# Performance work log

Hardware: AMD Instinct MI355X
Metric: run time of the kernel (lower is better)

## Reference

```python
import jax, jax.numpy as jnp
import numpy as np

D_IN = 1024
D_ATT = 1024
D_OUT = 1024
N, S = 8, 4096


def setup_inputs() -> dict:
    key = jax.random.key(0)
    ks = jax.random.split(key, 5)
    sc_in = 1.0 / np.sqrt(D_IN)
    sc_att = 1.0 / np.sqrt(D_ATT)
    return {
        "x": jax.random.normal(ks[0], (N, S, D_IN), dtype=jnp.float32),
        "Wq": jax.random.normal(ks[1], (D_IN, D_ATT), dtype=jnp.float32) * sc_in,
        "bq": jnp.zeros((D_ATT,), dtype=jnp.float32),
        "Wk": jax.random.normal(ks[2], (D_IN, D_ATT), dtype=jnp.float32) * sc_in,
        "bk": jnp.zeros((D_ATT,), dtype=jnp.float32),
        "Wv": jax.random.normal(ks[3], (D_IN, D_ATT), dtype=jnp.float32) * sc_in,
        "bv": jnp.zeros((D_ATT,), dtype=jnp.float32),
        "Wo": jax.random.normal(ks[4], (D_ATT, D_OUT), dtype=jnp.float32) * sc_att,
        "bo": jnp.zeros((D_OUT,), dtype=jnp.float32),
    }


def reference(x, Wq, bq, Wk, bk, Wv, bv, Wo, bo):
    # projections: [n, s, h]
    query = jnp.einsum('nsd,dh->nsh', x, Wq) + bq
    keyp = jnp.einsum('nsd,dh->nsh', x, Wk) + bk
    value = jnp.einsum('nsd,dh->nsh', x, Wv) + bv
    fmap = lambda t: jax.nn.elu(t) + 1.0
    Q = fmap(query)
    K = fmap(keyp)
    # per-channel reductions over sequence: [n, h]
    KV = jnp.sum(K * value, axis=1)
    Ksum = jnp.sum(K, axis=1)
    Z = 1.0 / (Q * Ksum[:, None, :] + 1e-6)  # [n, s, h]
    V = Q * KV[:, None, :] * Z  # [n, s, h]
    out = jnp.einsum('nsh,ho->nso', V, Wo) + bo
    return jax.nn.gelu(out)  # flax nn.gelu default approximate=True
```

## Files before the change

kernel.cpp:

```cpp
#include <hip/hip_runtime.h>
#include <hip/hip_bf16.h>

typedef __attribute__((ext_vector_type(8))) short bf16x8;
typedef __attribute__((ext_vector_type(4))) float f32x4;

#define GLOBAL_AS __attribute__((address_space(1)))
#define LDS_AS __attribute__((address_space(3)))

#define DCH 1024
#define SEQ 4096
#define NBATCH 8

static __device__ __forceinline__ unsigned int f2bf(float f) {
    unsigned int u = __float_as_uint(f);
    return (u + 0x7fffu + ((u >> 16) & 1u)) >> 16;
}

static __device__ __forceinline__ void async_copy16(const void* g, void* l) {
    __builtin_amdgcn_global_load_lds((const GLOBAL_AS void*)g, (LDS_AS void*)l, 16, 0, 0);
}

static __device__ __forceinline__ float gelu_tanh(float u) {
    float inner = 0.7978845608028654f * (u + 0.044715f * u * u * u);
    return 0.5f * u * (1.f + tanhf(inner));
}

__global__ __launch_bounds__(256) void prep_kernel(
    const float4* __restrict__ x, uint4* __restrict__ xb,
    const float* __restrict__ Wk, const float* __restrict__ Wv,
    unsigned short* __restrict__ WkT, unsigned short* __restrict__ WvT)
{
    __shared__ float tile[32][33];
    int tid = threadIdx.x;
    if (blockIdx.x < 16384) {
        size_t t = (size_t)blockIdx.x * 256 + tid;
        float4 f0 = x[t * 2], f1 = x[t * 2 + 1];
        uint4 a;
        a.x = f2bf(f0.x) | (f2bf(f0.y) << 16);
        a.y = f2bf(f0.z) | (f2bf(f0.w) << 16);
        a.z = f2bf(f1.x) | (f2bf(f1.y) << 16);
        a.w = f2bf(f1.z) | (f2bf(f1.w) << 16);
        xb[t] = a;
    } else {
        int b2 = blockIdx.x - 16384;
        const float* src = (b2 >> 10) ? Wv : Wk;
        unsigned short* dst = (b2 >> 10) ? WvT : WkT;
        int h0 = (b2 & 31) * 32, k0 = ((b2 >> 5) & 31) * 32;
        int tx = tid & 31, ty = tid >> 5;
#pragma unroll
        for (int i = 0; i < 4; i++)
            tile[ty + i * 8][tx] = src[(size_t)(k0 + ty + i * 8) * DCH + h0 + tx];
        __syncthreads();
#pragma unroll
        for (int i = 0; i < 4; i++)
            dst[(size_t)(h0 + ty + i * 8) * DCH + k0 + tx] =
                (unsigned short)f2bf(tile[tx][ty + i * 8]);
    }
}

__global__ __launch_bounds__(256) void wt_kernel(
    const float* __restrict__ Wk, const float* __restrict__ Wv,
    unsigned short* __restrict__ WkT, unsigned short* __restrict__ WvT)
{
    __shared__ float tile[32][33];
    const float* src = blockIdx.z ? Wv : Wk;
    unsigned short* dst = blockIdx.z ? WvT : WkT;
    int h0 = blockIdx.x * 32, k0 = blockIdx.y * 32;
    int tx = threadIdx.x, ty = threadIdx.y;
#pragma unroll
    for (int i = 0; i < 4; i++)
        tile[ty + i * 8][tx] = src[(size_t)(k0 + ty + i * 8) * DCH + h0 + tx];
    __syncthreads();
#pragma unroll
    for (int i = 0; i < 4; i++)
        dst[(size_t)(h0 + ty + i * 8) * DCH + k0 + tx] =
            (unsigned short)f2bf(tile[tx][ty + i * 8]);
}

__global__ __launch_bounds__(256) void kv_gemm_fast(
    const unsigned short* __restrict__ xb,
    const unsigned short* __restrict__ WkT,
    const unsigned short* __restrict__ WvT,
    const float* __restrict__ bk,
    const float* __restrict__ bv,
    float* __restrict__ part)
{
    __shared__ __align__(16) unsigned short sA[2][128 * 64];
    __shared__ __align__(16) unsigned short sK[2][64 * 64];
    __shared__ __align__(16) unsigned short sV[2][64 * 64];

    int b = blockIdx.x;
    int r = b & 7, j = b >> 3;
    int h_tile = j & 15;
    int ns = r * 32 + (j >> 4);
    int n = ns >> 5, s_tile = ns & 31;
    int s0 = s_tile * 128, h0 = h_tile * 64;

    int tid = threadIdx.x;
    int lane = tid & 63, wid = tid >> 6;
    int wsg = wid >> 1, wh = wid & 1;
    int col = lane & 15, lhi = lane >> 4;

    const unsigned short* gA[4];
    int aoff[4];
#pragma unroll
    for (int i = 0; i < 4; i++) {
        int c = (wid * 4 + i) * 64 + lane;
        int row = c >> 3, c8 = (c & 7) ^ (row & 7);
        gA[i] = xb + (size_t)(n * SEQ + s0 + row) * DCH + c8 * 8;
        aoff[i] = (wid * 4 + i) * 512;
    }
    const unsigned short* gK[2];
    const unsigned short* gV[2];
    int koff[2];
#pragma unroll
    for (int i = 0; i < 2; i++) {
        int c = (wid * 2 + i) * 64 + lane;
        int row = c >> 3, c8 = (c & 7) ^ (row & 7);
        gK[i] = WkT + (size_t)(h0 + row) * DCH + c8 * 8;
        gV[i] = WvT + (size_t)(h0 + row) * DCH + c8 * 8;
        koff[i] = (wid * 2 + i) * 512;
    }

    f32x4 acck[4][2], accv[4][2];
#pragma unroll
    for (int mt = 0; mt < 4; mt++)
#pragma unroll
        for (int nt = 0; nt < 2; nt++) {
            acck[mt][nt] = (f32x4){0.f, 0.f, 0.f, 0.f};
            accv[mt][nt] = (f32x4){0.f, 0.f, 0.f, 0.f};
        }

#pragma unroll
    for (int i = 0; i < 4; i++) async_copy16(gA[i], &sA[0][aoff[i]]);
#pragma unroll
    for (int i = 0; i < 2; i++) async_copy16(gK[i], &sK[0][koff[i]]);
#pragma unroll
    for (int i = 0; i < 2; i++) async_copy16(gV[i], &sV[0][koff[i]]);
    __syncthreads();

    int cur = 0;
    for (int kk = 0; kk < 16; kk++) {
        if (kk < 15) {
            int k0 = (kk + 1) * 64;
#pragma unroll
            for (int i = 0; i < 4; i++) async_copy16(gA[i] + k0, &sA[cur ^ 1][aoff[i]]);
#pragma unroll
            for (int i = 0; i < 2; i++) async_copy16(gK[i] + k0, &sK[cur ^ 1][koff[i]]);
#pragma unroll
            for (int i = 0; i < 2; i++) async_copy16(gV[i] + k0, &sV[cur ^ 1][koff[i]]);
        }
#pragma unroll
        for (int ks = 0; ks < 2; ks++) {
            bf16x8 af[4], bkf[2], bvf[2];
            int gg = ks * 4 + lhi;
#pragma unroll
            for (int mt = 0; mt < 4; mt++) {
                int rowa = wsg * 64 + mt * 16 + col;
                af[mt] = *((const bf16x8*)&sA[cur][rowa * 64 + ((gg ^ (rowa & 7)) * 8)]);
            }
#pragma unroll
            for (int nt = 0; nt < 2; nt++) {
                int rowb = wh * 32 + nt * 16 + col;
                int o = rowb * 64 + ((gg ^ (rowb & 7)) * 8);
                bkf[nt] = *((const bf16x8*)&sK[cur][o]);
                bvf[nt] = *((const bf16x8*)&sV[cur][o]);
            }
            __builtin_amdgcn_s_setprio(1);
#pragma unroll
            for (int mt = 0; mt < 4; mt++)
#pragma unroll
                for (int nt = 0; nt < 2; nt++) {
                    acck[mt][nt] = __builtin_amdgcn_mfma_f32_16x16x32_bf16(
                        af[mt], bkf[nt], acck[mt][nt], 0, 0, 0);
                    accv[mt][nt] = __builtin_amdgcn_mfma_f32_16x16x32_bf16(
                        af[mt], bvf[nt], accv[mt][nt], 0, 0, 0);
                }
            __builtin_amdgcn_s_setprio(0);
        }
        __syncthreads();
        cur ^= 1;
    }

    float* redf = (float*)&sA[0][0];

#pragma unroll
    for (int nt = 0; nt < 2; nt++) {
        int h_local = wh * 32 + nt * 16 + col;
        float bkv = bk[h0 + h_local];
        float bvv = bv[h0 + h_local];
        float pkv = 0.f, pks = 0.f;
#pragma unroll
        for (int mt = 0; mt < 4; mt++)
#pragma unroll
            for (int rr = 0; rr < 4; rr++) {
                float ck = acck[mt][nt][rr] + bkv;
                float cv = accv[mt][nt][rr] + bvv;
                float kq = ck > 0.f ? ck + 1.f : __expf(ck);
                pkv += kq * cv;
                pks += kq;
            }
        pkv += __shfl_xor(pkv, 16);
        pkv += __shfl_xor(pkv, 32);
        pks += __shfl_xor(pks, 16);
        pks += __shfl_xor(pks, 32);
        if (lhi == 0) {
            redf[(wsg * 64 + h_local) * 2 + 0] = pkv;
            redf[(wsg * 64 + h_local) * 2 + 1] = pks;
        }
    }
    __syncthreads();
    if (tid < 128) {
        int h = tid & 63, t = tid >> 6;
        float v = redf[(h) * 2 + t] + redf[(64 + h) * 2 + t];
        part[(((size_t)(n * 16 + h_tile) * 2 + t) * 32 + s_tile) * 64 + h] = v;
    }
}

__global__ __launch_bounds__(512) void kv_gemm_slow(
    const float* __restrict__ x,
    const unsigned short* __restrict__ WkT,
    const unsigned short* __restrict__ WvT,
    const float* __restrict__ bk,
    const float* __restrict__ bv,
    float* __restrict__ part)
{
    __shared__ unsigned short sA[128 * 64];
    __shared__ unsigned short sK[128 * 64];
    __shared__ unsigned short sV[128 * 64];
    __shared__ float red[2][128][2];

    int b = blockIdx.x;
    int r = b & 7, j = b >> 3;
    int ns = r * 32 + (j >> 3);
    int h_tile = j & 7;
    int n = ns >> 5, s_tile = ns & 31;
    int s0 = s_tile * 128, h0 = h_tile * 128;

    const float* xA = x + ((size_t)(n * SEQ + s0)) * DCH;

    int tid = threadIdx.x;
    int lane = tid & 63, wid = tid >> 6;
    int wsg = wid >> 2, wh = wid & 3;
    int col = lane & 15, lhi = lane >> 4;

    f32x4 acck[4][2], accv[4][2];
#pragma unroll
    for (int mt = 0; mt < 4; mt++)
#pragma unroll
        for (int nt = 0; nt < 2; nt++) {
            acck[mt][nt] = (f32x4){0.f, 0.f, 0.f, 0.f};
            accv[mt][nt] = (f32x4){0.f, 0.f, 0.f, 0.f};
        }

    for (int kk = 0; kk < 16; kk++) {
        int k0 = kk * 64;
#pragma unroll
        for (int i = 0; i < 2; i++) {
            int c = tid + i * 512;
            int row = c >> 3, c8 = c & 7;
            const float4* p = (const float4*)(xA + (size_t)row * DCH + k0 + c8 * 8);
            float4 f0 = p[0], f1 = p[1];
            unsigned int p0 = f2bf(f0.x) | (f2bf(f0.y) << 16);
            unsigned int p1 = f2bf(f0.z) | (f2bf(f0.w) << 16);
            unsigned int p2 = f2bf(f1.x) | (f2bf(f1.y) << 16);
            unsigned int p3 = f2bf(f1.z) | (f2bf(f1.w) << 16);
            uint4 pk = {p0, p1, p2, p3};
            int g = c8 ^ (row & 7);
            *((uint4*)&sA[row * 64 + g * 8]) = pk;
        }
#pragma unroll
        for (int i = 0; i < 2; i++) {
            int c = tid + i * 512;
            int row = c >> 3, c8 = c & 7;
            int g = c8 ^ (row & 7);
            *((uint4*)&sK[row * 64 + g * 8]) =
                *((const uint4*)(WkT + (size_t)(h0 + row) * DCH + k0 + c8 * 8));
            *((uint4*)&sV[row * 64 + g * 8]) =
                *((const uint4*)(WvT + (size_t)(h0 + row) * DCH + k0 + c8 * 8));
        }
        __syncthreads();
#pragma unroll
        for (int ks = 0; ks < 2; ks++) {
            bf16x8 af[4], bkf[2], bvf[2];
            int gg = ks * 4 + lhi;
#pragma unroll
            for (int mt = 0; mt < 4; mt++) {
                int rowa = wsg * 64 + mt * 16 + col;
                af[mt] = *((const bf16x8*)&sA[rowa * 64 + ((gg ^ (rowa & 7)) * 8)]);
            }
#pragma unroll
            for (int nt = 0; nt < 2; nt++) {
                int rowb = wh * 32 + nt * 16 + col;
                int o = rowb * 64 + ((gg ^ (rowb & 7)) * 8);
                bkf[nt] = *((const bf16x8*)&sK[o]);
                bvf[nt] = *((const bf16x8*)&sV[o]);
            }
#pragma unroll
            for (int mt = 0; mt < 4; mt++)
#pragma unroll
                for (int nt = 0; nt < 2; nt++) {
                    acck[mt][nt] = __builtin_amdgcn_mfma_f32_16x16x32_bf16(
                        af[mt], bkf[nt], acck[mt][nt], 0, 0, 0);
                    accv[mt][nt] = __builtin_amdgcn_mfma_f32_16x16x32_bf16(
                        af[mt], bvf[nt], accv[mt][nt], 0, 0, 0);
                }
        }
        __syncthreads();
    }

#pragma unroll
    for (int nt = 0; nt < 2; nt++) {
        int h_local = wh * 32 + nt * 16 + col;
        float bkv = bk[h0 + h_local];
        float bvv = bv[h0 + h_local];
        float pkv = 0.f, pks = 0.f;
#pragma unroll
        for (int mt = 0; mt < 4; mt++)
#pragma unroll
            for (int rr = 0; rr < 4; rr++) {
                float ck = acck[mt][nt][rr] + bkv;
                float cv = accv[mt][nt][rr] + bvv;
                float kq = ck > 0.f ? ck + 1.f : __expf(ck);
                pkv += kq * cv;
                pks += kq;
            }
        pkv += __shfl_xor(pkv, 16);
        pkv += __shfl_xor(pkv, 32);
        pks += __shfl_xor(pks, 16);
        pks += __shfl_xor(pks, 32);
        if (lhi == 0) {
            red[wsg][h_local][0] = pkv;
            red[wsg][h_local][1] = pks;
        }
    }
    __syncthreads();
    if (tid < 256) {
        int h = tid & 127, t = tid >> 7;
        float v = red[0][h][t] + red[1][h][t];
        int ht = h_tile * 2 + (h >> 6);
        part[(((size_t)(n * 16 + ht) * 2 + t) * 32 + s_tile) * 64 + (h & 63)] = v;
    }
}

__global__ __launch_bounds__(256) void out_part_kernel(
    const float* __restrict__ part, const float* __restrict__ Wo,
    float* __restrict__ part2)
{
    __shared__ float skv[128], sks[128], vs[128];
    int n = blockIdx.x, kc = blockIdx.y, ob = blockIdx.z;
    int tid = threadIdx.x;
    {
        int h = tid & 127, t = tid >> 7;
        int ht = kc * 2 + (h >> 6);
        const float* base = part + (((size_t)(n * 16 + ht) * 2 + t) * 32) * 64;
        float s = 0.f;
#pragma unroll 4
        for (int st = 0; st < 32; st++) s += base[st * 64 + (h & 63)];
        if (t == 0) skv[h] = s; else sks[h] = s;
    }
    __syncthreads();
    if (tid < 128) vs[tid] = skv[tid] / sks[tid];
    __syncthreads();
    int o = ob * 256 + tid;
    float acc = 0.f;
#pragma unroll 8
    for (int k = 0; k < 128; k++)
        acc += vs[k] * Wo[(size_t)(kc * 128 + k) * DCH + o];
    part2[(size_t)(n * 8 + kc) * DCH + o] = acc;
}

__global__ __launch_bounds__(256) void bcast_kernel(
    const float4* __restrict__ part2, const float4* __restrict__ bo,
    float4* __restrict__ out)
{
    int n = blockIdx.x >> 7;
    int sc = blockIdx.x & 127;
    int tid = threadIdx.x;
    float4 a = bo[tid];
#pragma unroll
    for (int kc = 0; kc < 8; kc++) {
        float4 p = part2[(size_t)(n * 8 + kc) * 256 + tid];
        a.x += p.x; a.y += p.y; a.z += p.z; a.w += p.w;
    }
    float4 v;
    v.x = gelu_tanh(a.x);
    v.y = gelu_tanh(a.y);
    v.z = gelu_tanh(a.z);
    v.w = gelu_tanh(a.w);
    size_t base = ((size_t)(n * SEQ) + (size_t)sc * 32) * 256 + tid;
#pragma unroll 4
    for (int s = 0; s < 32; s++)
        out[base + (size_t)s * 256] = v;
}

extern "C" void kernel_launch(void* const* d_in, const int* in_sizes, int n_in,
                              void* d_out, int out_size, void* d_ws, size_t ws_size,
                              hipStream_t stream) {
    const float* x  = (const float*)d_in[0];
    const float* Wk = (const float*)d_in[3];
    const float* bk = (const float*)d_in[4];
    const float* Wv = (const float*)d_in[5];
    const float* bv = (const float*)d_in[6];
    const float* Wo = (const float*)d_in[7];
    const float* bo = (const float*)d_in[8];

    const size_t XB_BYTES = (size_t)NBATCH * SEQ * DCH * 2;
    const size_t TAIL = (4u << 20) + (8u << 20) + (1u << 19);
    bool fast = ws_size >= XB_BYTES + TAIL;

    char* ws = (char*)d_ws;
    unsigned short* xb = (unsigned short*)ws;
    char* base = fast ? ws + XB_BYTES : ws;
    unsigned short* WkT = (unsigned short*)base;
    unsigned short* WvT = WkT + 1024 * 1024;
    float* part  = (float*)(base + 4 * 1024 * 1024);
    float* part2 = part + (size_t)8 * 16 * 2 * 32 * 64;

    if (fast) {
        prep_kernel<<<18432, 256, 0, stream>>>((const float4*)x, (uint4*)xb,
                                               Wk, Wv, WkT, WvT);
        kv_gemm_fast<<<4096, 256, 0, stream>>>(xb, WkT, WvT, bk, bv, part);
    } else {
        wt_kernel<<<dim3(32, 32, 2), dim3(32, 8), 0, stream>>>(Wk, Wv, WkT, WvT);
        kv_gemm_slow<<<2048, 512, 0, stream>>>(x, WkT, WvT, bk, bv, part);
    }
    out_part_kernel<<<dim3(8, 8, 4), 256, 0, stream>>>(part, Wo, part2);
    bcast_kernel<<<1024, 256, 0, stream>>>((const float4*)part2, (const float4*)bo,
                                           (float4*)d_out);
}
```

Before: 432.0 us.

## Enlarge KV GEMM tiles to 256x128 with a triple-buffered K-step-32 pipeline

Rewrites the fast K/V projection GEMM to use 512-thread blocks over 256x128 output tiles, so each block does more work and x and weight tiles are reused more. The K step drops to 32, with three LDS stages, explicit vmcnt waits and raw barriers, so two loads stay in flight while MFMAs run. The partial-sum layout now has 16 sequence tiles instead of 32, and out_part_kernel takes the tile count as a parameter. In exchange there is higher register pressure from 32 accumulators per wave and fewer blocks in the grid.

```diff
diff --git a/kernel.cpp b/kernel.cpp
--- a/kernel.cpp
+++ b/kernel.cpp
@@ -77,7 +77,7 @@
             (unsigned short)f2bf(tile[tx][ty + i * 8]);
 }
 
-__global__ __launch_bounds__(256) void kv_gemm_fast(
+__global__ __launch_bounds__(512, 2) void kv_gemm_fast(
     const unsigned short* __restrict__ xb,
     const unsigned short* __restrict__ WkT,
     const unsigned short* __restrict__ WvT,
@@ -85,46 +85,42 @@
     const float* __restrict__ bv,
     float* __restrict__ part)
 {
-    __shared__ __align__(16) unsigned short sA[2][128 * 64];
-    __shared__ __align__(16) unsigned short sK[2][64 * 64];
-    __shared__ __align__(16) unsigned short sV[2][64 * 64];
+    __shared__ __align__(16) unsigned short sA[3][256 * 32];
+    __shared__ __align__(16) unsigned short sK[3][128 * 32];
+    __shared__ __align__(16) unsigned short sV[3][128 * 32];
 
     int b = blockIdx.x;
     int r = b & 7, j = b >> 3;
-    int h_tile = j & 15;
-    int ns = r * 32 + (j >> 4);
-    int n = ns >> 5, s_tile = ns & 31;
-    int s0 = s_tile * 128, h0 = h_tile * 64;
+    int h_tile = j & 7;
+    int ns = r * 16 + (j >> 3);
+    int n = ns >> 4, s_tile = ns & 15;
+    int s0 = s_tile * 256, h0 = h_tile * 128;
 
     int tid = threadIdx.x;
     int lane = tid & 63, wid = tid >> 6;
-    int wsg = wid >> 1, wh = wid & 1;
+    int sg = wid >> 2, hg = wid & 3;
     int col = lane & 15, lhi = lane >> 4;
 
-    const unsigned short* gA[4];
-    int aoff[4];
-#pragma unroll
-    for (int i = 0; i < 4; i++) {
-        int c = (wid * 4 + i) * 64 + lane;
-        int row = c >> 3, c8 = (c & 7) ^ (row & 7);
+    const unsigned short* gA[2];
+#pragma unroll
+    for (int i = 0; i < 2; i++) {
+        int c = i * 512 + tid;
+        int row = c >> 2, c8 = (c & 3) ^ (row & 3);
         gA[i] = xb + (size_t)(n * SEQ + s0 + row) * DCH + c8 * 8;
-        aoff[i] = (wid * 4 + i) * 512;
-    }
-    const unsigned short* gK[2];
-    const unsigned short* gV[2];
-    int koff[2];
-#pragma unroll
-    for (int i = 0; i < 2; i++) {
-        int c = (wid * 2 + i) * 64 + lane;
-        int row = c >> 3, c8 = (c & 7) ^ (row & 7);
-        gK[i] = WkT + (size_t)(h0 + row) * DCH + c8 * 8;
-        gV[i] = WvT + (size_t)(h0 + row) * DCH + c8 * 8;
-        koff[i] = (wid * 2 + i) * 512;
-    }
-
-    f32x4 acck[4][2], accv[4][2];
-#pragma unroll
-    for (int mt = 0; mt < 4; mt++)
+    }
+    const unsigned short* gK;
+    const unsigned short* gV;
+    {
+        int c = tid;
+        int row = c >> 2, c8 = (c & 3) ^ (row & 3);
+        gK = WkT + (size_t)(h0 + row) * DCH + c8 * 8;
+        gV = WvT + (size_t)(h0 + row) * DCH + c8 * 8;
+    }
+    int aBase = wid * 64 * 8;
+
+    f32x4 acck[8][2], accv[8][2];
+#pragma unroll
+    for (int mt = 0; mt < 8; mt++)
 #pragma unroll
         for (int nt = 0; nt < 2; nt++) {
             acck[mt][nt] = (f32x4){0.f, 0.f, 0.f, 0.f};
@@ -132,66 +128,79 @@
         }
 
 #pragma unroll
-    for (int i = 0; i < 4; i++) async_copy16(gA[i], &sA[0][aoff[i]]);
-#pragma unroll
-    for (int i = 0; i < 2; i++) async_copy16(gK[i], &sK[0][koff[i]]);
-#pragma unroll
-    for (int i = 0; i < 2; i++) async_copy16(gV[i], &sV[0][koff[i]]);
-    __syncthreads();
-
-    int cur = 0;
-    for (int kk = 0; kk < 16; kk++) {
-        if (kk < 15) {
-            int k0 = (kk + 1) * 64;
-#pragma unroll
-            for (int i = 0; i < 4; i++) async_copy16(gA[i] + k0, &sA[cur ^ 1][aoff[i]]);
-#pragma unroll
-            for (int i = 0; i < 2; i++) async_copy16(gK[i] + k0, &sK[cur ^ 1][koff[i]]);
-#pragma unroll
-            for (int i = 0; i < 2; i++) async_copy16(gV[i] + k0, &sV[cur ^ 1][koff[i]]);
-        }
-#pragma unroll
-        for (int ks = 0; ks < 2; ks++) {
-            bf16x8 af[4], bkf[2], bvf[2];
-            int gg = ks * 4 + lhi;
-#pragma unroll
-            for (int mt = 0; mt < 4; mt++) {
-                int rowa = wsg * 64 + mt * 16 + col;
-                af[mt] = *((const bf16x8*)&sA[cur][rowa * 64 + ((gg ^ (rowa & 7)) * 8)]);
+    for (int t0 = 0; t0 < 2; t0++) {
+        int k0 = t0 * 32;
+#pragma unroll
+        for (int i = 0; i < 2; i++)
+            async_copy16(gA[i] + k0, &sA[t0][i * 512 * 8 + aBase]);
+        async_copy16(gK + k0, &sK[t0][aBase]);
+        async_copy16(gV + k0, &sV[t0][aBase]);
+    }
+    asm volatile("s_waitcnt vmcnt(4)" ::: "memory");
+    __builtin_amdgcn_sched_barrier(0);
+    __builtin_amdgcn_s_barrier();
+    __builtin_amdgcn_sched_barrier(0);
+
+    int q = 0;
+    for (int t = 0; t < 32; t++) {
+        int w = q + 2 >= 3 ? q - 1 : q + 2;
+        if (t < 30) {
+            int k0 = (t + 2) * 32;
+#pragma unroll
+            for (int i = 0; i < 2; i++)
+                async_copy16(gA[i] + k0, &sA[w][i * 512 * 8 + aBase]);
+            async_copy16(gK + k0, &sK[w][aBase]);
+            async_copy16(gV + k0, &sV[w][aBase]);
+        }
+        bf16x8 af[8], bkf[2], bvf[2];
+#pragma unroll
+        for (int mt = 0; mt < 8; mt++) {
+            int rowa = sg * 128 + mt * 16 + col;
+            af[mt] = *((const bf16x8*)&sA[q][rowa * 32 + ((lhi ^ (rowa & 3)) * 8)]);
+        }
+#pragma unroll
+        for (int nt = 0; nt < 2; nt++) {
+            int rowb = hg * 32 + nt * 16 + col;
+            int o = rowb * 32 + ((lhi ^ (rowb & 3)) * 8);
+            bkf[nt] = *((const bf16x8*)&sK[q][o]);
+            bvf[nt] = *((const bf16x8*)&sV[q][o]);
+        }
+        __builtin_amdgcn_s_setprio(1);
+#pragma unroll
+        for (int mt = 0; mt < 8; mt++)
+#pragma unroll
+            for (int nt = 0; nt < 2; nt++) {
+                acck[mt][nt] = __builtin_amdgcn_mfma_f32_16x16x32_bf16(
+                    af[mt], bkf[nt], acck[mt][nt], 0, 0, 0);
+                accv[mt][nt] = __builtin_amdgcn_mfma_f32_16x16x32_bf16(
+                    af[mt], bvf[nt], accv[mt][nt], 0, 0, 0);
             }
-#pragma unroll
-            for (int nt = 0; nt < 2; nt++) {
-                int rowb = wh * 32 + nt * 16 + col;
-                int o = rowb * 64 + ((gg ^ (rowb & 7)) * 8);
-                bkf[nt] = *((const bf16x8*)&sK[cur][o]);
-                bvf[nt] = *((const bf16x8*)&sV[cur][o]);
-            }
-            __builtin_amdgcn_s_setprio(1);
-#pragma unroll
-            for (int mt = 0; mt < 4; mt++)
-#pragma unroll
-                for (int nt = 0; nt < 2; nt++) {
-                    acck[mt][nt] = __builtin_amdgcn_mfma_f32_16x16x32_bf16(
-                        af[mt], bkf[nt], acck[mt][nt], 0, 0, 0);
-                    accv[mt][nt] = __builtin_amdgcn_mfma_f32_16x16x32_bf16(
-                        af[mt], bvf[nt], accv[mt][nt], 0, 0, 0);
-                }
-            __builtin_amdgcn_s_setprio(0);
-        }
-        __syncthreads();
-        cur ^= 1;
+        __builtin_amdgcn_s_setprio(0);
+
+        if (t < 30) {
+            asm volatile("s_waitcnt vmcnt(4)" ::: "memory");
+            __builtin_amdgcn_sched_barrier(0);
+            __builtin_amdgcn_s_barrier();
+            __builtin_amdgcn_sched_barrier(0);
+        } else if (t == 30) {
+            asm volatile("s_waitcnt vmcnt(0)" ::: "memory");
+            __builtin_amdgcn_sched_barrier(0);
+            __builtin_amdgcn_s_barrier();
+            __builtin_amdgcn_sched_barrier(0);
+        }
+        q = q + 1 >= 3 ? 0 : q + 1;
     }
 
     float* redf = (float*)&sA[0][0];
 
 #pragma unroll
     for (int nt = 0; nt < 2; nt++) {
-        int h_local = wh * 32 + nt * 16 + col;
+        int h_local = hg * 32 + nt * 16 + col;
         float bkv = bk[h0 + h_local];
         float bvv = bv[h0 + h_local];
         float pkv = 0.f, pks = 0.f;
 #pragma unroll
-        for (int mt = 0; mt < 4; mt++)
+        for (int mt = 0; mt < 8; mt++)
 #pragma unroll
             for (int rr = 0; rr < 4; rr++) {
                 float ck = acck[mt][nt][rr] + bkv;
@@ -205,15 +214,16 @@
         pks += __shfl_xor(pks, 16);
         pks += __shfl_xor(pks, 32);
         if (lhi == 0) {
-            redf[(wsg * 64 + h_local) * 2 + 0] = pkv;
-            redf[(wsg * 64 + h_local) * 2 + 1] = pks;
+            redf[(sg * 128 + h_local) * 2 + 0] = pkv;
+            redf[(sg * 128 + h_local) * 2 + 1] = pks;
         }
     }
     __syncthreads();
-    if (tid < 128) {
-        int h = tid & 63, t = tid >> 6;
-        float v = redf[(h) * 2 + t] + redf[(64 + h) * 2 + t];
-        part[(((size_t)(n * 16 + h_tile) * 2 + t) * 32 + s_tile) * 64 + h] = v;
+    if (tid < 256) {
+        int h = tid & 127, t2 = tid >> 7;
+        float v = redf[h * 2 + t2] + redf[(128 + h) * 2 + t2];
+        int ht = h_tile * 2 + (h >> 6);
+        part[(((size_t)(n * 16 + ht) * 2 + t2) * 16 + s_tile) * 64 + (h & 63)] = v;
     }
 }
 
@@ -345,7 +355,7 @@
 
 __global__ __launch_bounds__(256) void out_part_kernel(
     const float* __restrict__ part, const float* __restrict__ Wo,
-    float* __restrict__ part2)
+    float* __restrict__ part2, int nst)
 {
     __shared__ float skv[128], sks[128], vs[128];
     int n = blockIdx.x, kc = blockIdx.y, ob = blockIdx.z;
@@ -353,10 +363,10 @@
     {
         int h = tid & 127, t = tid >> 7;
         int ht = kc * 2 + (h >> 6);
-        const float* base = part + (((size_t)(n * 16 + ht) * 2 + t) * 32) * 64;
+        const float* base = part + (((size_t)(n * 16 + ht) * 2 + t) * nst) * 64;
         float s = 0.f;
 #pragma unroll 4
-        for (int st = 0; st < 32; st++) s += base[st * 64 + (h & 63)];
+        for (int st = 0; st < nst; st++) s += base[st * 64 + (h & 63)];
         if (t == 0) skv[h] = s; else sks[h] = s;
     }
     __syncthreads();
@@ -420,12 +430,13 @@
     if (fast) {
         prep_kernel<<<18432, 256, 0, stream>>>((const float4*)x, (uint4*)xb,
                                                Wk, Wv, WkT, WvT);
-        kv_gemm_fast<<<4096, 256, 0, stream>>>(xb, WkT, WvT, bk, bv, part);
+        kv_gemm_fast<<<1024, 512, 0, stream>>>(xb, WkT, WvT, bk, bv, part);
+        out_part_kernel<<<dim3(8, 8, 4), 256, 0, stream>>>(part, Wo, part2, 16);
     } else {
         wt_kernel<<<dim3(32, 32, 2), dim3(32, 8), 0, stream>>>(Wk, Wv, WkT, WvT);
         kv_gemm_slow<<<2048, 512, 0, stream>>>(x, WkT, WvT, bk, bv, part);
-    }
-    out_part_kernel<<<dim3(8, 8, 4), 256, 0, stream>>>(part, Wo, part2);
+        out_part_kernel<<<dim3(8, 8, 4), 256, 0, stream>>>(part, Wo, part2, 32);
+    }
     bcast_kernel<<<1024, 256, 0, stream>>>((const float4*)part2, (const float4*)bo,
                                            (float4*)d_out);
 }
```

After: 437.4 us. Within noise of the previous version (+1.3%).
